# Optimization experiments

Measured on AMD Instinct MI355X. Metric: run time of the kernel, lower is better.

The kernel has to match this reference:

```python
import jax, jax.numpy as jnp
import numpy as np

B, TQ, TK, D, H = 4, 2048, 2048, 512, 8  # hidden=512, num_heads=8, head_dim=64


def setup_inputs() -> dict:
    key = jax.random.key(0)
    ks = jax.random.split(key, 7)
    s = 0.03  # small init scale for linear weights
    return {
        "q": jax.random.normal(ks[0], (B, TQ, D), jnp.float32),
        "k": jax.random.normal(ks[1], (B, TK, D), jnp.float32),
        "v": jax.random.normal(ks[2], (B, TK, D), jnp.float32),
        "Wq": jax.random.normal(ks[3], (D, D), jnp.float32) * s,
        "bq": jnp.zeros((D,), jnp.float32),
        "Wk": jax.random.normal(ks[4], (D, D), jnp.float32) * s,
        "bk": jnp.zeros((D,), jnp.float32),
        "Wv": jax.random.normal(ks[5], (D, D), jnp.float32) * s,
        "bv": jnp.zeros((D,), jnp.float32),
        "Wo": jax.random.normal(ks[6], (D, D), jnp.float32) * s,
        "bo": jnp.zeros((D,), jnp.float32),
    }


def reference(q, k, v, Wq, bq, Wk, bk, Wv, bv, Wo, bo):
    Bq, Tq, _ = q.shape
    Tk = k.shape[1]
    Dh = D // H  # head dim = 64
    # torch Linear: x @ W.T + b; split heads -> [B, H, T, Dh]
    qh = (q @ Wq.T + bq).reshape(Bq, Tq, H, Dh).transpose(0, 2, 1, 3)
    kh = (k @ Wk.T + bk).reshape(Bq, Tk, H, Dh).transpose(0, 2, 1, 3)
    vh = (v @ Wv.T + bv).reshape(Bq, Tk, H, Dh).transpose(0, 2, 1, 3)
    scale = 1.0 / float(np.sqrt(Dh))
    scores = jnp.einsum("bhqd,bhkd->bhqk", qh, kh) * scale  # [B,H,Tq,Tk]
    # causal mask: tril(ones, diagonal=Tk-Tq); log-additive masking == -inf off-band
    causal = jnp.tril(jnp.ones((Tq, Tk), bool), k=Tk - Tq)
    scores = jnp.where(causal, scores, -jnp.inf)
    w = jax.nn.softmax(scores, axis=-1)  # attention weights
    x = jnp.einsum("bhqk,bhkd->bhqd", w, vh)
    x = x.transpose(0, 2, 1, 3).reshape(Bq, Tq, D)
    return x @ Wo.T + bo, w
```

## Files before the change

### kernel.cpp

```cpp
#include <hip/hip_runtime.h>


typedef __attribute__((ext_vector_type(4))) float f32x4;
typedef __attribute__((ext_vector_type(8))) short short8;
typedef __attribute__((ext_vector_type(8))) __bf16 bf16x8;
typedef __attribute__((ext_vector_type(2))) unsigned int uintx2;

static __device__ __forceinline__ unsigned short f2bf(float f) {
  unsigned u = __builtin_bit_cast(unsigned, f);
  u += 0x7fffu + ((u >> 16) & 1u);
  return (unsigned short)(u >> 16);
}

static __device__ __forceinline__ f32x4 mfma16(short8 a, short8 b, f32x4 c) {
  return __builtin_amdgcn_mfma_f32_16x16x32_bf16(
      __builtin_bit_cast(bf16x8, a), __builtin_bit_cast(bf16x8, b), c, 0, 0, 0);
}

#define GLD16(gsrc, ldst)                                                     \
  __builtin_amdgcn_global_load_lds(                                           \
      (const __attribute__((address_space(1))) void*)(gsrc),                  \
      (__attribute__((address_space(3))) void*)(ldst), 16, 0, 0)

template <int IN_BF16>
__device__ __forceinline__ void gemm_core(const void* __restrict__ Xv,
                                          const float* __restrict__ W,
                                          short (*As)[72], short (*Bs)[72],
                                          int row0, int col0, f32x4 (&acc)[4][4]) {
  const int tid = threadIdx.x;
  const int lane = tid & 63;
  const int wv = tid >> 6, wm = wv >> 1, wn = wv & 1;
  const int g = lane >> 4, c = lane & 15;

  for (int k0 = 0; k0 < 512; k0 += 64) {
    for (int ch = tid; ch < 1024; ch += 256) {
      const int r = ch >> 3, kc = (ch & 7) * 8;
      if (IN_BF16) {
        *(short8*)&As[r][kc] =
            *(const short8*)((const short*)Xv + (size_t)(row0 + r) * 512 + k0 + kc);
      } else {
        const float* src = (const float*)Xv + (size_t)(row0 + r) * 512 + k0 + kc;
        const f32x4 f0 = *(const f32x4*)src;
        const f32x4 f1 = *(const f32x4*)(src + 4);
        short8 s;
#pragma unroll
        for (int i = 0; i < 4; ++i) { s[i] = (short)f2bf(f0[i]); s[4 + i] = (short)f2bf(f1[i]); }
        *(short8*)&As[r][kc] = s;
      }
      {
        const float* src = W + (size_t)(col0 + r) * 512 + k0 + kc;
        const f32x4 f0 = *(const f32x4*)src;
        const f32x4 f1 = *(const f32x4*)(src + 4);
        short8 s;
#pragma unroll
        for (int i = 0; i < 4; ++i) { s[i] = (short)f2bf(f0[i]); s[4 + i] = (short)f2bf(f1[i]); }
        *(short8*)&Bs[r][kc] = s;
      }
    }
    __syncthreads();
#pragma unroll
    for (int kk = 0; kk < 2; ++kk) {
      short8 a[4], b[4];
#pragma unroll
      for (int i = 0; i < 4; ++i) a[i] = *(const short8*)&As[wm * 64 + i * 16 + c][kk * 32 + g * 8];
#pragma unroll
      for (int i = 0; i < 4; ++i) b[i] = *(const short8*)&Bs[wn * 64 + i * 16 + c][kk * 32 + g * 8];
#pragma unroll
      for (int mi = 0; mi < 4; ++mi)
#pragma unroll
        for (int ni = 0; ni < 4; ++ni) acc[mi][ni] = mfma16(a[mi], b[ni], acc[mi][ni]);
    }
    __syncthreads();
  }
}

__global__ __launch_bounds__(256) void qkv_gemm(
    const float* __restrict__ q, const float* __restrict__ k, const float* __restrict__ v,
    const float* __restrict__ Wq, const float* __restrict__ bq,
    const float* __restrict__ Wk, const float* __restrict__ bk,
    const float* __restrict__ Wv, const float* __restrict__ bv,
    unsigned short* __restrict__ Qbf, unsigned short* __restrict__ Kbf,
    unsigned short* __restrict__ Vbf) {
  __shared__ short As[128][72];
  __shared__ short Bs[128][72];
  const int z = blockIdx.z;
  const float* X = z == 0 ? q : (z == 1 ? k : v);
  const float* W = z == 0 ? Wq : (z == 1 ? Wk : Wv);
  const float* bias = z == 0 ? bq : (z == 1 ? bk : bv);
  const int row0 = blockIdx.x * 128, col0 = blockIdx.y * 128;

  f32x4 acc[4][4] = {};
  gemm_core<0>(X, W, As, Bs, row0, col0, acc);

  const int lane = threadIdx.x & 63;
  const int wv = threadIdx.x >> 6, wm = wv >> 1, wn = wv & 1;
  const int g = lane >> 4, c = lane & 15;

  if (z < 2) {
    unsigned short* Y = z == 0 ? Qbf : Kbf;
#pragma unroll
    for (int mi = 0; mi < 4; ++mi)
#pragma unroll
      for (int ni = 0; ni < 4; ++ni) {
        const int col = col0 + wn * 64 + ni * 16 + c;
        const float bvl = bias[col];
        const int rowb = row0 + wm * 64 + mi * 16 + g * 4;
#pragma unroll
        for (int r = 0; r < 4; ++r) {
          const int row = rowb + r;
          const int bb = row >> 11, t = row & 2047;
          const int h = col >> 6, dh = col & 63;
          Y[((size_t)((bb * 8 + h) * 2048 + t) << 6) + dh] = f2bf(acc[mi][ni][r] + bvl);
        }
      }
  } else {
#pragma unroll
    for (int mi = 0; mi < 4; ++mi)
#pragma unroll
      for (int ni = 0; ni < 4; ++ni) {
        const int col = col0 + wn * 64 + ni * 16 + c;
        const float bvl = bias[col];
        const int rowb = row0 + wm * 64 + mi * 16 + g * 4;
        const int bb = rowb >> 11, t = rowb & 2047;
        const int h = col >> 6, dh = col & 63;
        unsigned short w0 = f2bf(acc[mi][ni][0] + bvl), w1 = f2bf(acc[mi][ni][1] + bvl);
        unsigned short w2 = f2bf(acc[mi][ni][2] + bvl), w3 = f2bf(acc[mi][ni][3] + bvl);
        uintx2 pk;
        pk[0] = (unsigned)w0 | ((unsigned)w1 << 16);
        pk[1] = (unsigned)w2 | ((unsigned)w3 << 16);
        *(uintx2*)(Vbf + ((size_t)((bb * 8 + h) * 64 + dh) * 2048 + t)) = pk;
      }
  }
}

__global__ __launch_bounds__(256) void out_gemm(const unsigned short* __restrict__ ctx,
                                                const float* __restrict__ Wo,
                                                const float* __restrict__ bo,
                                                float* __restrict__ out) {
  __shared__ short As[128][72];
  __shared__ short Bs[128][72];
  const int row0 = blockIdx.x * 128, col0 = blockIdx.y * 128;
  f32x4 acc[4][4] = {};
  gemm_core<1>(ctx, Wo, As, Bs, row0, col0, acc);

  const int lane = threadIdx.x & 63;
  const int wv = threadIdx.x >> 6, wm = wv >> 1, wn = wv & 1;
  const int g = lane >> 4, c = lane & 15;
#pragma unroll
  for (int mi = 0; mi < 4; ++mi)
#pragma unroll
    for (int ni = 0; ni < 4; ++ni) {
      const int col = col0 + wn * 64 + ni * 16 + c;
      const float bvl = bo[col];
      const int rowb = row0 + wm * 64 + mi * 16 + g * 4;
#pragma unroll
      for (int r = 0; r < 4; ++r) out[(size_t)(rowb + r) * 512 + col] = acc[mi][ni][r] + bvl;
    }
}

__global__ __launch_bounds__(256) void attn_kernel(
    const unsigned short* __restrict__ Qb, const unsigned short* __restrict__ Kb,
    const unsigned short* __restrict__ Vtg, unsigned short* __restrict__ ctx,
    float* __restrict__ wout) {
  __shared__ short Ks[8192];
  __shared__ short Vs[8192];
  __shared__ short Ps[4][16][136];

  const int tid = threadIdx.x, lane = tid & 63, wv = tid >> 6;
  const int g = lane >> 4, c = lane & 15;
  const int p = blockIdx.x, bh = blockIdx.y;
  const unsigned short* Qp = Qb + (size_t)bh * (2048 * 64);
  const unsigned short* Kp = Kb + (size_t)bh * (2048 * 64);
  const unsigned short* Vp = Vtg + (size_t)bh * (64 * 2048);
  const int b_ = bh >> 3, h_ = bh & 7;

  for (int half = 0; half < 2; ++half) {
    const int t = half ? (31 - p) : p;
    const int q0 = t * 64;
    const int jmax = t >> 1;
    const int qr = q0 + wv * 16 + c;

    short8 qf[2];
    qf[0] = *(const short8*)(Qp + (size_t)qr * 64 + g * 8);
    qf[1] = *(const short8*)(Qp + (size_t)qr * 64 + 32 + g * 8);

    f32x4 O[4] = {};
    float m_r = -3.0e38f, l_r = 0.0f;

    for (int j = 0; j <= jmax; ++j) {
      __syncthreads();
#pragma unroll
      for (int i = 0; i < 4; ++i) {
        const int gr = (wv * 4 + i) * 64 + lane;
        const int row = gr >> 3, slot = gr & 7;
        GLD16(Kp + ((size_t)(j * 128 + row) * 64) + ((slot ^ (row & 7)) << 3),
              (char*)Ks + ((wv * 4 + i) << 10));
      }
#pragma unroll
      for (int i = 0; i < 4; ++i) {
        const int gr = (wv * 4 + i) * 64 + lane;
        const int row = gr >> 4, slot = gr & 15;
        GLD16(Vp + ((size_t)row * 2048) + j * 128 + ((slot ^ (row & 7)) << 3),
              (char*)Vs + ((wv * 4 + i) << 10));
      }
      __syncthreads();

      f32x4 S[8];
#pragma unroll
      for (int nc = 0; nc < 8; ++nc) S[nc] = (f32x4){0.f, 0.f, 0.f, 0.f};
#pragma unroll
      for (int kk = 0; kk < 2; ++kk)
#pragma unroll
        for (int nc = 0; nc < 8; ++nc) {
          const int row = nc * 16 + c;
          const short8 kf = *(const short8*)&Ks[row * 64 + (((kk * 4 + g) ^ (c & 7)) << 3)];
          S[nc] = mfma16(kf, qf[kk], S[nc]);
        }

#pragma unroll
      for (int nc = 0; nc < 8; ++nc) S[nc] *= 0.125f;
      if (j == jmax) {
        const int kvb = j * 128 + g * 4;
#pragma unroll
        for (int nc = 0; nc < 8; ++nc)
#pragma unroll
          for (int r = 0; r < 4; ++r)
            if (kvb + nc * 16 + r > qr) S[nc][r] = -1.0e30f;
      }

      float mx = -1.0e30f;
#pragma unroll
      for (int nc = 0; nc < 8; ++nc)
#pragma unroll
        for (int r = 0; r < 4; ++r) mx = fmaxf(mx, S[nc][r]);
      mx = fmaxf(mx, __shfl_xor(mx, 16));
      mx = fmaxf(mx, __shfl_xor(mx, 32));
      const float mn = fmaxf(m_r, mx);
      const float sc = __expf(m_r - mn);
      m_r = mn;
      float sum = 0.f;
#pragma unroll
      for (int nc = 0; nc < 8; ++nc)
#pragma unroll
        for (int r = 0; r < 4; ++r) {
          const float pv = __expf(S[nc][r] - mn);
          S[nc][r] = pv;
          sum += pv;
        }
      sum += __shfl_xor(sum, 16);
      sum += __shfl_xor(sum, 32);
      l_r = l_r * sc + sum;

      float scr[4];
#pragma unroll
      for (int r = 0; r < 4; ++r) scr[r] = __shfl(sc, g * 4 + r);
#pragma unroll
      for (int nd = 0; nd < 4; ++nd) {
        O[nd][0] *= scr[0]; O[nd][1] *= scr[1]; O[nd][2] *= scr[2]; O[nd][3] *= scr[3];
      }

#pragma unroll
      for (int nc = 0; nc < 8; ++nc) {
        uintx2 pk;
        pk[0] = (unsigned)f2bf(S[nc][0]) | ((unsigned)f2bf(S[nc][1]) << 16);
        pk[1] = (unsigned)f2bf(S[nc][2]) | ((unsigned)f2bf(S[nc][3]) << 16);
        *(uintx2*)&Ps[wv][c][nc * 16 + g * 4] = pk;
      }

#pragma unroll
      for (int kk2 = 0; kk2 < 4; ++kk2) {
        const short8 pa = *(const short8*)&Ps[wv][c][kk2 * 32 + g * 8];
#pragma unroll
        for (int nd = 0; nd < 4; ++nd) {
          const int row = nd * 16 + c;
          const short8 vb = *(const short8*)&Vs[row * 128 + (((kk2 * 4 + g) ^ (c & 7)) << 3)];
          O[nd] = mfma16(pa, vb, O[nd]);
        }
      }
    }

    {
      float lv[4];
#pragma unroll
      for (int r = 0; r < 4; ++r) lv[r] = __shfl(l_r, g * 4 + r);
#pragma unroll
      for (int r = 0; r < 4; ++r) {
        const float inv = 1.0f / lv[r];
        const int trow = q0 + wv * 16 + g * 4 + r;
        unsigned short* cp = ctx + ((size_t)(b_ * 2048 + trow) * 512) + h_ * 64;
#pragma unroll
        for (int nd = 0; nd < 4; ++nd) cp[nd * 16 + c] = f2bf(O[nd][r] * inv);
      }
    }

    const float inv_l = 1.0f / l_r;
    float* wbase = wout + ((size_t)bh * 2048 + q0) * 2048;
    for (int j = jmax; j >= 0; --j) {
      if (j != jmax) {
        __syncthreads();
#pragma unroll
        for (int i = 0; i < 4; ++i) {
          const int gr = (wv * 4 + i) * 64 + lane;
          const int row = gr >> 3, slot = gr & 7;
          GLD16(Kp + ((size_t)(j * 128 + row) * 64) + ((slot ^ (row & 7)) << 3),
                (char*)Ks + ((wv * 4 + i) << 10));
        }
        __syncthreads();
      }

      f32x4 S[8];
#pragma unroll
      for (int nc = 0; nc < 8; ++nc) S[nc] = (f32x4){0.f, 0.f, 0.f, 0.f};
#pragma unroll
      for (int kk = 0; kk < 2; ++kk)
#pragma unroll
        for (int nc = 0; nc < 8; ++nc) {
          const int row = nc * 16 + c;
          const short8 kf = *(const short8*)&Ks[row * 64 + (((kk * 4 + g) ^ (c & 7)) << 3)];
          S[nc] = mfma16(kf, qf[kk], S[nc]);
        }

      const bool lastj = (j == jmax);
      float* wr = wbase + (size_t)(wv * 16 + c) * 2048 + j * 128;
#pragma unroll
      for (int nc = 0; nc < 8; ++nc) {
        f32x4 w4;
#pragma unroll
        for (int r = 0; r < 4; ++r) {
          float val = __expf(S[nc][r] * 0.125f - m_r) * inv_l;
          if (lastj && (j * 128 + nc * 16 + g * 4 + r > qr)) val = 0.f;
          w4[r] = val;
        }
        *(f32x4*)(wr + nc * 16 + g * 4) = w4;
      }
    }

    {
      const int c0 = (jmax + 1) * 128;
      const f32x4 z = {0.f, 0.f, 0.f, 0.f};
      for (int rr = wv; rr < 64; rr += 4) {
        float* rp = wbase + (size_t)rr * 2048;
        for (int x = c0 + lane * 4; x < 2048; x += 256) *(f32x4*)(rp + x) = z;
      }
    }
  }
}

extern "C" void kernel_launch(void* const* d_in, const int* in_sizes, int n_in,
                              void* d_out, int out_size, void* d_ws, size_t ws_size,
                              hipStream_t stream) {
  const float* q  = (const float*)d_in[0];
  const float* k  = (const float*)d_in[1];
  const float* v  = (const float*)d_in[2];
  const float* Wq = (const float*)d_in[3];
  const float* bq = (const float*)d_in[4];
  const float* Wk = (const float*)d_in[5];
  const float* bk = (const float*)d_in[6];
  const float* Wv = (const float*)d_in[7];
  const float* bv = (const float*)d_in[8];
  const float* Wo = (const float*)d_in[9];
  const float* bo = (const float*)d_in[10];

  unsigned short* Qbf = (unsigned short*)d_ws;
  unsigned short* Kbf = Qbf + (size_t)4194304;
  unsigned short* Vbf = Kbf + (size_t)4194304;
  unsigned short* ctx = Vbf + (size_t)4194304;

  float* out  = (float*)d_out;
  float* wout = out + (size_t)4 * 2048 * 512;

  qkv_gemm<<<dim3(64, 4, 3), 256, 0, stream>>>(q, k, v, Wq, bq, Wk, bk, Wv, bv, Qbf, Kbf, Vbf);
  attn_kernel<<<dim3(16, 32), 256, 0, stream>>>(Qbf, Kbf, Vbf, ctx, wout);
  out_gemm<<<dim3(64, 4), 256, 0, stream>>>(ctx, Wo, bo, out);
}
```

Before: 243.1 us.

## Double-buffer K/V tiles in attention and use exp2 with hardware bf16 conversion

The attention kernel now keeps two LDS buffers for K and V. It prefetches the next tile asynchronously while computing on the current one, which cuts the per-iteration barrier pair to a single barrier in both the forward pass and the weight-writing pass. Softmax now uses exp2 with the log2(e)/sqrt(d) scale folded into the score multiply. The P scratch buffer is XOR-swizzled instead of padded, and float-to-bf16 conversion uses the compiler's native cast instead of a manual rounding routine. The cost is doubled K/V LDS usage, which may lower occupancy.

```diff
diff --git a/kernel.cpp b/kernel.cpp
--- a/kernel.cpp
+++ b/kernel.cpp
@@ -5,11 +5,21 @@
 typedef __attribute__((ext_vector_type(8))) short short8;
 typedef __attribute__((ext_vector_type(8))) __bf16 bf16x8;
 typedef __attribute__((ext_vector_type(2))) unsigned int uintx2;
-
-static __device__ __forceinline__ unsigned short f2bf(float f) {
-  unsigned u = __builtin_bit_cast(unsigned, f);
-  u += 0x7fffu + ((u >> 16) & 1u);
-  return (unsigned short)(u >> 16);
+typedef __attribute__((ext_vector_type(4))) unsigned int uintx4;
+
+static __device__ __forceinline__ unsigned short bfc(float f) {
+  return __builtin_bit_cast(unsigned short, (__bf16)f);
+}
+static __device__ __forceinline__ unsigned pkbf(float a, float b) {
+  return (unsigned)bfc(a) | ((unsigned)bfc(b) << 16);
+}
+static __device__ __forceinline__ short8 cvt_bf8(f32x4 f0, f32x4 f1) {
+  uintx4 u;
+  u[0] = pkbf(f0[0], f0[1]);
+  u[1] = pkbf(f0[2], f0[3]);
+  u[2] = pkbf(f1[0], f1[1]);
+  u[3] = pkbf(f1[2], f1[3]);
+  return __builtin_bit_cast(short8, u);
 }
 
 static __device__ __forceinline__ f32x4 mfma16(short8 a, short8 b, f32x4 c) {
@@ -40,21 +50,11 @@
             *(const short8*)((const short*)Xv + (size_t)(row0 + r) * 512 + k0 + kc);
       } else {
         const float* src = (const float*)Xv + (size_t)(row0 + r) * 512 + k0 + kc;
-        const f32x4 f0 = *(const f32x4*)src;
-        const f32x4 f1 = *(const f32x4*)(src + 4);
-        short8 s;
-#pragma unroll
-        for (int i = 0; i < 4; ++i) { s[i] = (short)f2bf(f0[i]); s[4 + i] = (short)f2bf(f1[i]); }
-        *(short8*)&As[r][kc] = s;
+        *(short8*)&As[r][kc] = cvt_bf8(*(const f32x4*)src, *(const f32x4*)(src + 4));
       }
       {
         const float* src = W + (size_t)(col0 + r) * 512 + k0 + kc;
-        const f32x4 f0 = *(const f32x4*)src;
-        const f32x4 f1 = *(const f32x4*)(src + 4);
-        short8 s;
-#pragma unroll
-        for (int i = 0; i < 4; ++i) { s[i] = (short)f2bf(f0[i]); s[4 + i] = (short)f2bf(f1[i]); }
-        *(short8*)&Bs[r][kc] = s;
+        *(short8*)&Bs[r][kc] = cvt_bf8(*(const f32x4*)src, *(const f32x4*)(src + 4));
       }
     }
     __syncthreads();
@@ -110,7 +110,7 @@
           const int row = rowb + r;
           const int bb = row >> 11, t = row & 2047;
           const int h = col >> 6, dh = col & 63;
-          Y[((size_t)((bb * 8 + h) * 2048 + t) << 6) + dh] = f2bf(acc[mi][ni][r] + bvl);
+          Y[((size_t)((bb * 8 + h) * 2048 + t) << 6) + dh] = bfc(acc[mi][ni][r] + bvl);
         }
       }
   } else {
@@ -123,11 +123,9 @@
         const int rowb = row0 + wm * 64 + mi * 16 + g * 4;
         const int bb = rowb >> 11, t = rowb & 2047;
         const int h = col >> 6, dh = col & 63;
-        unsigned short w0 = f2bf(acc[mi][ni][0] + bvl), w1 = f2bf(acc[mi][ni][1] + bvl);
-        unsigned short w2 = f2bf(acc[mi][ni][2] + bvl), w3 = f2bf(acc[mi][ni][3] + bvl);
         uintx2 pk;
-        pk[0] = (unsigned)w0 | ((unsigned)w1 << 16);
-        pk[1] = (unsigned)w2 | ((unsigned)w3 << 16);
+        pk[0] = pkbf(acc[mi][ni][0] + bvl, acc[mi][ni][1] + bvl);
+        pk[1] = pkbf(acc[mi][ni][2] + bvl, acc[mi][ni][3] + bvl);
         *(uintx2*)(Vbf + ((size_t)((bb * 8 + h) * 64 + dh) * 2048 + t)) = pk;
       }
   }
@@ -162,17 +160,19 @@
     const unsigned short* __restrict__ Qb, const unsigned short* __restrict__ Kb,
     const unsigned short* __restrict__ Vtg, unsigned short* __restrict__ ctx,
     float* __restrict__ wout) {
-  __shared__ short Ks[8192];
-  __shared__ short Vs[8192];
-  __shared__ short Ps[4][16][136];
+  __shared__ short Kd[2][8192];
+  __shared__ short Vd[2][8192];
+  __shared__ short Ps[4][16][128];
 
   const int tid = threadIdx.x, lane = tid & 63, wv = tid >> 6;
   const int g = lane >> 4, c = lane & 15;
+  const int sw = (c & 7) << 3;
   const int p = blockIdx.x, bh = blockIdx.y;
   const unsigned short* Qp = Qb + (size_t)bh * (2048 * 64);
   const unsigned short* Kp = Kb + (size_t)bh * (2048 * 64);
   const unsigned short* Vp = Vtg + (size_t)bh * (64 * 2048);
   const int b_ = bh >> 3, h_ = bh & 7;
+  const float SCALE = 0.18033688f;
 
   for (int half = 0; half < 2; ++half) {
     const int t = half ? (31 - p) : p;
@@ -180,6 +180,22 @@
     const int jmax = t >> 1;
     const int qr = q0 + wv * 16 + c;
 
+    __syncthreads();
+#pragma unroll
+    for (int i = 0; i < 4; ++i) {
+      const int gr = (wv * 4 + i) * 64 + lane;
+      const int row = gr >> 3, slot = gr & 7;
+      GLD16(Kp + ((size_t)row * 64) + ((slot ^ (row & 7)) << 3),
+            (char*)Kd[0] + ((wv * 4 + i) << 10));
+    }
+#pragma unroll
+    for (int i = 0; i < 4; ++i) {
+      const int gr = (wv * 4 + i) * 64 + lane;
+      const int row = gr >> 4, slot = gr & 15;
+      GLD16(Vp + ((size_t)row * 2048) + ((slot ^ (row & 7)) << 3),
+            (char*)Vd[0] + ((wv * 4 + i) << 10));
+    }
+
     short8 qf[2];
     qf[0] = *(const short8*)(Qp + (size_t)qr * 64 + g * 8);
     qf[1] = *(const short8*)(Qp + (size_t)qr * 64 + 32 + g * 8);
@@ -189,21 +205,25 @@
 
     for (int j = 0; j <= jmax; ++j) {
       __syncthreads();
-#pragma unroll
-      for (int i = 0; i < 4; ++i) {
-        const int gr = (wv * 4 + i) * 64 + lane;
-        const int row = gr >> 3, slot = gr & 7;
-        GLD16(Kp + ((size_t)(j * 128 + row) * 64) + ((slot ^ (row & 7)) << 3),
-              (char*)Ks + ((wv * 4 + i) << 10));
-      }
-#pragma unroll
-      for (int i = 0; i < 4; ++i) {
-        const int gr = (wv * 4 + i) * 64 + lane;
-        const int row = gr >> 4, slot = gr & 15;
-        GLD16(Vp + ((size_t)row * 2048) + j * 128 + ((slot ^ (row & 7)) << 3),
-              (char*)Vs + ((wv * 4 + i) << 10));
-      }
-      __syncthreads();
+      if (j < jmax) {
+        const int nb = (j + 1) & 1;
+#pragma unroll
+        for (int i = 0; i < 4; ++i) {
+          const int gr = (wv * 4 + i) * 64 + lane;
+          const int row = gr >> 3, slot = gr & 7;
+          GLD16(Kp + ((size_t)((j + 1) * 128 + row) * 64) + ((slot ^ (row & 7)) << 3),
+                (char*)Kd[nb] + ((wv * 4 + i) << 10));
+        }
+#pragma unroll
+        for (int i = 0; i < 4; ++i) {
+          const int gr = (wv * 4 + i) * 64 + lane;
+          const int row = gr >> 4, slot = gr & 15;
+          GLD16(Vp + ((size_t)row * 2048) + (j + 1) * 128 + ((slot ^ (row & 7)) << 3),
+                (char*)Vd[nb] + ((wv * 4 + i) << 10));
+        }
+      }
+      const short* Ksb = Kd[j & 1];
+      const short* Vsb = Vd[j & 1];
 
       f32x4 S[8];
 #pragma unroll
@@ -213,12 +233,12 @@
 #pragma unroll
         for (int nc = 0; nc < 8; ++nc) {
           const int row = nc * 16 + c;
-          const short8 kf = *(const short8*)&Ks[row * 64 + (((kk * 4 + g) ^ (c & 7)) << 3)];
+          const short8 kf = *(const short8*)&Ksb[row * 64 + (((kk * 4 + g) ^ (c & 7)) << 3)];
           S[nc] = mfma16(kf, qf[kk], S[nc]);
         }
 
 #pragma unroll
-      for (int nc = 0; nc < 8; ++nc) S[nc] *= 0.125f;
+      for (int nc = 0; nc < 8; ++nc) S[nc] *= SCALE;
       if (j == jmax) {
         const int kvb = j * 128 + g * 4;
 #pragma unroll
@@ -236,14 +256,14 @@
       mx = fmaxf(mx, __shfl_xor(mx, 16));
       mx = fmaxf(mx, __shfl_xor(mx, 32));
       const float mn = fmaxf(m_r, mx);
-      const float sc = __expf(m_r - mn);
+      const float sc = __builtin_amdgcn_exp2f(m_r - mn);
       m_r = mn;
       float sum = 0.f;
 #pragma unroll
       for (int nc = 0; nc < 8; ++nc)
 #pragma unroll
         for (int r = 0; r < 4; ++r) {
-          const float pv = __expf(S[nc][r] - mn);
+          const float pv = __builtin_amdgcn_exp2f(S[nc][r] - mn);
           S[nc][r] = pv;
           sum += pv;
         }
@@ -262,18 +282,18 @@
 #pragma unroll
       for (int nc = 0; nc < 8; ++nc) {
         uintx2 pk;
-        pk[0] = (unsigned)f2bf(S[nc][0]) | ((unsigned)f2bf(S[nc][1]) << 16);
-        pk[1] = (unsigned)f2bf(S[nc][2]) | ((unsigned)f2bf(S[nc][3]) << 16);
-        *(uintx2*)&Ps[wv][c][nc * 16 + g * 4] = pk;
+        pk[0] = pkbf(S[nc][0], S[nc][1]);
+        pk[1] = pkbf(S[nc][2], S[nc][3]);
+        *(uintx2*)&Ps[wv][c][(nc * 16 + g * 4) ^ sw] = pk;
       }
 
 #pragma unroll
       for (int kk2 = 0; kk2 < 4; ++kk2) {
-        const short8 pa = *(const short8*)&Ps[wv][c][kk2 * 32 + g * 8];
+        const short8 pa = *(const short8*)&Ps[wv][c][(kk2 * 32 + g * 8) ^ sw];
 #pragma unroll
         for (int nd = 0; nd < 4; ++nd) {
           const int row = nd * 16 + c;
-          const short8 vb = *(const short8*)&Vs[row * 128 + (((kk2 * 4 + g) ^ (c & 7)) << 3)];
+          const short8 vb = *(const short8*)&Vsb[row * 128 + (((kk2 * 4 + g) ^ (c & 7)) << 3)];
           O[nd] = mfma16(pa, vb, O[nd]);
         }
       }
@@ -289,24 +309,24 @@
         const int trow = q0 + wv * 16 + g * 4 + r;
         unsigned short* cp = ctx + ((size_t)(b_ * 2048 + trow) * 512) + h_ * 64;
 #pragma unroll
-        for (int nd = 0; nd < 4; ++nd) cp[nd * 16 + c] = f2bf(O[nd][r] * inv);
+        for (int nd = 0; nd < 4; ++nd) cp[nd * 16 + c] = bfc(O[nd][r] * inv);
       }
     }
 
     const float inv_l = 1.0f / l_r;
     float* wbase = wout + ((size_t)bh * 2048 + q0) * 2048;
     for (int j = jmax; j >= 0; --j) {
-      if (j != jmax) {
-        __syncthreads();
+      __syncthreads();
+      if (j > 0) {
 #pragma unroll
         for (int i = 0; i < 4; ++i) {
           const int gr = (wv * 4 + i) * 64 + lane;
           const int row = gr >> 3, slot = gr & 7;
-          GLD16(Kp + ((size_t)(j * 128 + row) * 64) + ((slot ^ (row & 7)) << 3),
-                (char*)Ks + ((wv * 4 + i) << 10));
-        }
-        __syncthreads();
-      }
+          GLD16(Kp + ((size_t)((j - 1) * 128 + row) * 64) + ((slot ^ (row & 7)) << 3),
+                (char*)Kd[(j - 1) & 1] + ((wv * 4 + i) << 10));
+        }
+      }
+      const short* Ksb = Kd[j & 1];
 
       f32x4 S[8];
 #pragma unroll
@@ -316,7 +336,7 @@
 #pragma unroll
         for (int nc = 0; nc < 8; ++nc) {
           const int row = nc * 16 + c;
-          const short8 kf = *(const short8*)&Ks[row * 64 + (((kk * 4 + g) ^ (c & 7)) << 3)];
+          const short8 kf = *(const short8*)&Ksb[row * 64 + (((kk * 4 + g) ^ (c & 7)) << 3)];
           S[nc] = mfma16(kf, qf[kk], S[nc]);
         }
 
@@ -327,7 +347,7 @@
         f32x4 w4;
 #pragma unroll
         for (int r = 0; r < 4; ++r) {
-          float val = __expf(S[nc][r] * 0.125f - m_r) * inv_l;
+          float val = __builtin_amdgcn_exp2f(S[nc][r] * SCALE - m_r) * inv_l;
           if (lastj && (j * 128 + nc * 16 + g * 4 + r > qr)) val = 0.f;
           w4[r] = val;
         }
```

Result: no change. 241.1 us (-0.8%).
